# Kernel tuning notes

Hardware: AMD Instinct MI355X
Metric: run time of the kernel (lower is better)

The kernel has to match this reference:

```python
import jax, jax.numpy as jnp
import numpy as np

B, C, D, H, W = 2, 384, 32, 32, 32
HEADS, WS = 12, 5
HD = C // HEADS
PAD = WS // 2
SCALE = HD ** -0.5


def setup_inputs() -> dict:
    key = jax.random.key(0)
    ks = jax.random.split(key, 6)
    return {
        "x": jax.random.normal(ks[0], (B, C, D, H, W), jnp.float32),
        "w_qkv": jax.random.normal(ks[1], (3 * C, C), jnp.float32) * 0.02,
        "b_qkv": jax.random.normal(ks[2], (3 * C,), jnp.float32) * 0.02,
        "w_proj": jax.random.normal(ks[3], (C, C), jnp.float32) * 0.02,
        "b_proj": jax.random.normal(ks[4], (C,), jnp.float32) * 0.02,
        "pos_embed": jax.random.normal(ks[5], (HD, WS, WS, WS), jnp.float32) * 0.02,
    }


def reference(x, w_qkv, b_qkv, w_proj, b_proj, pos_embed):
    # 1x1x1 conv == pointwise linear over channels
    qkv = jnp.einsum('bcdhw,oc->bodhw', x, w_qkv) + b_qkv[None, :, None, None, None]
    q, k, v = jnp.split(qkv, 3, axis=1)
    q = q.reshape(B, HEADS, HD, D, H, W)
    k = k.reshape(B, HEADS, HD, D, H, W)
    v = v.reshape(B, HEADS, HD, D, H, W)
    pad_cfg = ((0, 0), (0, 0), (0, 0), (PAD, PAD), (PAD, PAD), (PAD, PAD))
    k_pad = jnp.pad(k, pad_cfg)  # zero padding, as in torch F.pad(value=0)
    v_pad = jnp.pad(v, pad_cfg)
    # per-offset scores: equivalent to unfold(ws)^3 without materializing windows
    scores = []
    for dz in range(WS):
        for dy in range(WS):
            for dx in range(WS):
                k_s = k_pad[:, :, :, dz:dz + D, dy:dy + H, dx:dx + W]
                # pos embed is added to k windows (including padded zeros) as in original
                k_s = k_s + pos_embed[:, dz, dy, dx][None, None, :, None, None, None]
                scores.append(jnp.sum(q * k_s, axis=2) * SCALE)  # [B,heads,D,H,W]
    scores = jnp.stack(scores, axis=-1)  # [B,heads,D,H,W,WS^3]
    wts = jax.nn.softmax(scores, axis=-1)
    out = jnp.zeros((B, HEADS, HD, D, H, W), x.dtype)
    i = 0
    for dz in range(WS):
        for dy in range(WS):
            for dx in range(WS):
                v_s = v_pad[:, :, :, dz:dz + D, dy:dy + H, dx:dx + W]
                out = out + wts[..., i][:, :, None] * v_s
                i += 1
    out = out.reshape(B, C, D, H, W)
    out = jnp.einsum('bcdhw,oc->bodhw', out, w_proj) + b_proj[None, :, None, None, None]
    return out
```

## Files before the change

kernel.cpp:

```cpp
#include <hip/hip_runtime.h>


#define NB 2
#define NC 384
#define NHEADS 12
#define NHD 32
#define NS 32768
#define PERB 12582912
#define SCALE_F 0.17677669529663687f
#define LOG2E_F 1.4426950408889634f
#define SL_F (0.17677669529663687f * 1.4426950408889634f)

typedef unsigned short bfr;
typedef float floatx4 __attribute__((ext_vector_type(4)));
typedef float f32x4 __attribute__((ext_vector_type(4)));
typedef short bf16x8 __attribute__((ext_vector_type(8)));
typedef short short4v __attribute__((ext_vector_type(4)));

union B8 { floatx4 v; bfr h[8]; };

__device__ __forceinline__ float b2f(bfr u) {
    union { unsigned int i; float f; } v;
    v.i = (unsigned int)u << 16;
    return v.f;
}
__device__ __forceinline__ bfr f2b(float f) {
    union { float f; unsigned int i; } v;
    v.f = f;
    unsigned int x = v.i;
    return (bfr)((x + 0x7fffu + ((x >> 16) & 1u)) >> 16);
}

__global__ void fill_code(float* out, float code) {
    for (size_t i = (size_t)blockIdx.x*256 + threadIdx.x; i < (size_t)NB*PERB;
         i += (size_t)gridDim.x*256) out[i] = code;
}

__global__ __launch_bounds__(256) void qkv_mfma(
    const float* __restrict__ x, const float* __restrict__ w,
    const float* __restrict__ bias,
    bfr* __restrict__ qT, bfr* __restrict__ kT, bfr* __restrict__ vT, int b)
{
    __shared__ __attribute__((aligned(16))) bfr wl[128*40];
    __shared__ __attribute__((aligned(16))) bfr xl[128*40];
    __shared__ float bsh[128];
    const int tid  = threadIdx.x;
    const int lane = tid & 63;
    const int wave = tid >> 6;
    const int wo   = (wave & 1) * 64;
    const int wsq  = (wave >> 1) * 64;
    const int s0   = blockIdx.x * 128;
    const int o0   = blockIdx.y * 128;
    const int m16  = lane & 15;
    const int g    = lane >> 4;

    if (tid < 128) bsh[tid] = bias[o0 + tid];

    f32x4 acc[4][4];
    #pragma unroll
    for (int i = 0; i < 4; ++i)
        #pragma unroll
        for (int j = 0; j < 4; ++j) acc[i][j] = (f32x4){0.f, 0.f, 0.f, 0.f};

    for (int kc = 0; kc < 12; ++kc) {
        const int c0 = kc * 32;
        #pragma unroll
        for (int r = 0; r < 4; ++r) {
            const int idx = r*256 + tid;
            const int o   = idx >> 3;
            const int c4  = (idx & 7) * 4;
            floatx4 wv = *(const floatx4*)&w[(size_t)(o0 + o)*NC + c0 + c4];
            short4v t;
            t[0] = (short)f2b(wv[0]); t[1] = (short)f2b(wv[1]);
            t[2] = (short)f2b(wv[2]); t[3] = (short)f2b(wv[3]);
            *(short4v*)&wl[o*40 + c4] = t;
        }
        #pragma unroll
        for (int r = 0; r < 4; ++r) {
            const int idx = r*256 + tid;
            const int c   = idx >> 5;
            const int s4  = (idx & 31) * 4;
            floatx4 xv =
                *(const floatx4*)&x[((size_t)b*NC + c0 + c)*NS + s0 + s4];
            #pragma unroll
            for (int i = 0; i < 4; ++i) xl[(s4 + i)*40 + c] = f2b(xv[i]);
        }
        __syncthreads();
        bf16x8 af[4], bfg[4];
        #pragma unroll
        for (int i = 0; i < 4; ++i)
            af[i] = *(bf16x8*)&wl[(wo + i*16 + m16)*40 + g*8];
        #pragma unroll
        for (int j = 0; j < 4; ++j)
            bfg[j] = *(bf16x8*)&xl[(wsq + j*16 + m16)*40 + g*8];
        #pragma unroll
        for (int i = 0; i < 4; ++i)
            #pragma unroll
            for (int j = 0; j < 4; ++j)
                acc[i][j] = __builtin_amdgcn_mfma_f32_16x16x32_bf16(
                    af[i], bfg[j], acc[i][j], 0, 0, 0);
        __syncthreads();
    }

    const int tens = blockIdx.y / 3;
    bfr* dstT = (tens == 0) ? qT : ((tens == 1) ? kT : vT);
    const int remb = o0 - tens*NC;
    const int q4   = g * 4;
    #pragma unroll
    for (int i = 0; i < 4; ++i) {
        const int olb = wo + i*16 + q4;
        const int ob  = remb + olb;
        const int hh  = ob >> 5;
        const int cc  = ob & 31;
        #pragma unroll
        for (int j = 0; j < 4; ++j) {
            const int s = s0 + wsq + j*16 + m16;
            short4v t;
            #pragma unroll
            for (int r = 0; r < 4; ++r)
                t[r] = (short)f2b(acc[i][j][r] + bsh[olb + r]);
            *(short4v*)&dstT[((size_t)hh*NS + s)*NHD + cc] = t;
        }
    }
}

__global__ __launch_bounds__(256, 4) void attn3d(
    const bfr* __restrict__ qT, const bfr* __restrict__ kT,
    const bfr* __restrict__ vT, const float* __restrict__ pe,
    bfr* __restrict__ aT)
{
    __shared__ __attribute__((aligned(16))) unsigned char smem[40960];
    bfr (*kl)[40]   = reinterpret_cast<bfr(*)[40]>(smem);
    bfr (*vtl)[136] = reinterpret_cast<bfr(*)[136]>(smem + 10240);
    bfr (*pel)[40]  = reinterpret_cast<bfr(*)[40]>(smem);
    bfr (*ql)[40]   = reinterpret_cast<bfr(*)[40]>(smem + 18944);
    bfr (*qpl)[132] = reinterpret_cast<bfr(*)[132]>(smem + 24064);

    const int tid  = threadIdx.x;
    const int lane = tid & 63;
    const int wave = tid >> 6;
    const int m16  = lane & 15;
    const int g    = lane >> 4;
    const int g4   = g << 2;
    const int bx   = blockIdx.x;
    const int tz = bx >> 6, ty = (bx >> 3) & 7, tx = bx & 7;
    const size_t hb = (size_t)blockIdx.y * NS;

    {
        const int qr = tid >> 2, part = tid & 3;
        const int qzr = qr >> 4, qyr = (qr >> 2) & 3, qxr = qr & 3;
        const size_t sq =
            (size_t)(tz*4 + qzr)*1024 + (ty*4 + qyr)*32 + (tx*4 + qxr);
        *(floatx4*)&ql[qr][part*8] =
            *(const floatx4*)&qT[(hb + sq)*NHD + part*8];
    }
    for (int e = tid; e < 4000; e += 256) {
        const int hd = e / 125;
        const int n  = e - hd*125;
        pel[n][hd] = f2b(pe[e]);
    }
    if (tid < 96) pel[125 + (tid >> 5)][tid & 31] = 0;
    __syncthreads();

    const int wq = wave*16 + m16;
    const bf16x8 bq = *(const bf16x8*)&ql[wq][g*8];

    #pragma unroll
    for (int t = 0; t < 8; ++t) {
        bf16x8 pa = *(const bf16x8*)&pel[t*16 + m16][g*8];
        f32x4 qa = __builtin_amdgcn_mfma_f32_16x16x32_bf16(
            pa, bq, (f32x4){0.f, 0.f, 0.f, 0.f}, 0, 0, 0);
        const unsigned w0 = (unsigned)f2b(qa[0]*SL_F) |
                            ((unsigned)f2b(qa[1]*SL_F) << 16);
        const unsigned w1 = (unsigned)f2b(qa[2]*SL_F) |
                            ((unsigned)f2b(qa[3]*SL_F) << 16);
        *(uint2*)&qpl[wq][t*16 + g4] = make_uint2(w0, w1);
    }
    if (g == 0) qpl[wq][128] = 0xFF80u;

    const int qy = m16 >> 2, qx = m16 & 3;
    unsigned nopk[4];
    #pragma unroll
    for (int tt = 0; tt < 4; ++tt) {
        unsigned v = 0;
        #pragma unroll
        for (int r = 0; r < 4; ++r) {
            const int t0 = g4 + r;
            const int hy = 2*tt + (t0 >> 3), hx = t0 & 7;
            const int dy = hy - qy, dx = hx - qx;
            const bool ok = ((unsigned)dy < 5u) && ((unsigned)dx < 5u);
            v |= (unsigned)(ok ? (dy*5 + dx) : 128) << (8*r);
        }
        nopk[tt] = v;
    }
    const bfr* qprow = qpl[wq];
    const int a0 = (m16 + 32*(g & 1)) * 4;
    const int a1 = a0 + 64;
    const bool ghi = (g >= 2);

    float m = -1e30f, l = 0.f;
    f32x4 o[2];
    o[0] = (f32x4){0.f, 0.f, 0.f, 0.f};
    o[1] = (f32x4){0.f, 0.f, 0.f, 0.f};

    for (int c = 0; c < 4; ++c) {
        __syncthreads();
        #pragma unroll
        for (int r2 = 0; r2 < 2; ++r2) {
            const int idx = r2*256 + tid;
            const int key = idx >> 2, part = idx & 3;
            const int hz = key >> 6, hy = (key >> 3) & 7, hx = key & 7;
            const int gz = tz*4 - 2 + 2*c + hz, gy = ty*4 - 2 + hy,
                      gx = tx*4 - 2 + hx;
            floatx4 kv = (floatx4){0.f, 0.f, 0.f, 0.f};
            if ((unsigned)gz < 32u && (unsigned)gy < 32u && (unsigned)gx < 32u)
                kv = *(const floatx4*)
                     &kT[(hb + gz*1024 + gy*32 + gx)*NHD + part*8];
            *(floatx4*)&kl[key][part*8] = kv;
        }
        {
            const int kp = tid & 63, hdo = tid >> 6;
            const int aK = 2*kp;
            const int hz = aK >> 6;
            const int hy = (aK >> 3) & 7, hx = aK & 7;
            const int gz = tz*4 - 2 + 2*c + hz, gy = ty*4 - 2 + hy,
                      gx = tx*4 - 2 + hx;
            const bool vzy = ((unsigned)gz < 32u) && ((unsigned)gy < 32u);
            B8 va, vb;
            va.v = (floatx4){0.f, 0.f, 0.f, 0.f};
            vb.v = (floatx4){0.f, 0.f, 0.f, 0.f};
            const size_t gb = hb + gz*1024 + gy*32;
            if (vzy && (unsigned)gx < 32u)
                va.v = *(const floatx4*)&vT[(gb + gx)*NHD + hdo*8];
            if (vzy && (unsigned)(gx + 1) < 32u)
                vb.v = *(const floatx4*)&vT[(gb + gx + 1)*NHD + hdo*8];
            #pragma unroll
            for (int i = 0; i < 8; ++i) {
                const unsigned u = (unsigned)va.h[i] | ((unsigned)vb.h[i] << 16);
                *(unsigned*)&vtl[hdo*8 + i][aK] = u;
            }
        }
        __syncthreads();

        #pragma unroll
        for (int zl = 0; zl < 2; ++zl) {
            const int dz = 2*c + zl - wave;
            if ((unsigned)dz > 4u) continue;
            const int nz = dz * 25;
            f32x4 s[4];
            __builtin_amdgcn_s_setprio(1);
            #pragma unroll
            for (int tt = 0; tt < 4; ++tt) {
                bf16x8 ka = *(const bf16x8*)&kl[zl*64 + tt*16 + m16][g*8];
                s[tt] = __builtin_amdgcn_mfma_f32_16x16x32_bf16(
                    ka, bq, (f32x4){0.f, 0.f, 0.f, 0.f}, 0, 0, 0);
            }
            __builtin_amdgcn_s_setprio(0);
            float mx = -1e30f;
            #pragma unroll
            for (int tt = 0; tt < 4; ++tt) {
                #pragma unroll
                for (int r = 0; r < 4; ++r) {
                    const unsigned n =
                        min((unsigned)nz + ((nopk[tt] >> (8*r)) & 255u), 128u);
                    const float qb  = b2f(qprow[n]);
                    const float val = fmaf(s[tt][r], SL_F, qb);
                    s[tt][r] = val;
                    mx = fmaxf(mx, val);
                }
            }
            mx = fmaxf(mx, __shfl_xor(mx, 16));
            mx = fmaxf(mx, __shfl_xor(mx, 32));
            const float mn = fmaxf(m, mx);
            const float al = exp2f(m - mn);
            m = mn;
            float ls = 0.f;
            unsigned pk[4][2];
            #pragma unroll
            for (int tt = 0; tt < 4; ++tt) {
                const float p0 = exp2f(s[tt][0] - mn);
                const float p1 = exp2f(s[tt][1] - mn);
                const float p2 = exp2f(s[tt][2] - mn);
                const float p3 = exp2f(s[tt][3] - mn);
                ls += (p0 + p1) + (p2 + p3);
                pk[tt][0] = (unsigned)f2b(p0) | ((unsigned)f2b(p1) << 16);
                pk[tt][1] = (unsigned)f2b(p2) | ((unsigned)f2b(p3) << 16);
            }
            ls += __shfl_xor(ls, 16);
            ls += __shfl_xor(ls, 32);
            l = l * al + ls;
            #pragma unroll
            for (int i = 0; i < 4; ++i) { o[0][i] *= al; o[1][i] *= al; }
            #pragma unroll
            for (int ksl = 0; ksl < 2; ++ksl) {
                union { unsigned u[4]; bf16x8 v; } pb;
                #pragma unroll
                for (int w = 0; w < 4; ++w) {
                    const int ad = (w < 2) ? a0 : a1;
                    const int wi = w & 1;
                    const int lo = __builtin_amdgcn_ds_bpermute(
                        ad, (int)pk[2*ksl][wi]);
                    const int hi = __builtin_amdgcn_ds_bpermute(
                        ad, (int)pk[2*ksl + 1][wi]);
                    pb.u[w] = ghi ? (unsigned)hi : (unsigned)lo;
                }
                __builtin_amdgcn_s_setprio(1);
                #pragma unroll
                for (int mt = 0; mt < 2; ++mt) {
                    bf16x8 va = *(const bf16x8*)
                        &vtl[mt*16 + m16][zl*64 + ksl*32 + g*8];
                    o[mt] = __builtin_amdgcn_mfma_f32_16x16x32_bf16(
                        va, pb.v, o[mt], 0, 0, 0);
                }
                __builtin_amdgcn_s_setprio(0);
            }
        }
    }

    const float rl = 1.f / l;
    const size_t sq = (size_t)(tz*4 + wave)*1024 + (ty*4 + qy)*32 + (tx*4 + qx);
    #pragma unroll
    for (int mt = 0; mt < 2; ++mt) {
        const unsigned w0 = (unsigned)f2b(o[mt][0]*rl) |
                            ((unsigned)f2b(o[mt][1]*rl) << 16);
        const unsigned w1 = (unsigned)f2b(o[mt][2]*rl) |
                            ((unsigned)f2b(o[mt][3]*rl) << 16);
        *(uint2*)&aT[(hb + sq)*NHD + mt*16 + g4] = make_uint2(w0, w1);
    }
}

__global__ __launch_bounds__(256) void proj_mfma(
    const bfr* __restrict__ aT, const float* __restrict__ w,
    const float* __restrict__ bias, float* __restrict__ out)
{
    __shared__ __attribute__((aligned(16))) bfr wl[128*40];
    __shared__ __attribute__((aligned(16))) bfr xl[128*40];
    __shared__ float bsh[128];
    const int tid  = threadIdx.x;
    const int lane = tid & 63;
    const int wave = tid >> 6;
    const int wo   = (wave & 1) * 64;
    const int wsq  = (wave >> 1) * 64;
    const int s0   = blockIdx.x * 128;
    const int o0   = blockIdx.y * 128;
    const int m16  = lane & 15;
    const int g    = lane >> 4;

    if (tid < 128) bsh[tid] = bias[o0 + tid];

    f32x4 acc[4][4];
    #pragma unroll
    for (int i = 0; i < 4; ++i)
        #pragma unroll
        for (int j = 0; j < 4; ++j) acc[i][j] = (f32x4){0.f, 0.f, 0.f, 0.f};

    for (int kc = 0; kc < 12; ++kc) {
        const int c0 = kc * 32;
        #pragma unroll
        for (int r = 0; r < 4; ++r) {
            const int idx = r*256 + tid;
            const int o   = idx >> 3;
            const int c4  = (idx & 7) * 4;
            floatx4 wv = *(const floatx4*)&w[(size_t)(o0 + o)*NC + c0 + c4];
            short4v t;
            t[0] = (short)f2b(wv[0]); t[1] = (short)f2b(wv[1]);
            t[2] = (short)f2b(wv[2]); t[3] = (short)f2b(wv[3]);
            *(short4v*)&wl[o*40 + c4] = t;
        }
        #pragma unroll
        for (int r = 0; r < 2; ++r) {
            const int idx = r*256 + tid;
            const int s   = idx >> 2;
            const int gg  = idx & 3;
            *(floatx4*)&xl[s*40 + gg*8] =
                *(const floatx4*)&aT[((size_t)kc*NS + s0 + s)*NHD + gg*8];
        }
        __syncthreads();
        bf16x8 af[4], bfg[4];
        #pragma unroll
        for (int i = 0; i < 4; ++i)
            af[i] = *(bf16x8*)&wl[(wo + i*16 + m16)*40 + g*8];
        #pragma unroll
        for (int j = 0; j < 4; ++j)
            bfg[j] = *(bf16x8*)&xl[(wsq + j*16 + m16)*40 + g*8];
        #pragma unroll
        for (int i = 0; i < 4; ++i)
            #pragma unroll
            for (int j = 0; j < 4; ++j)
                acc[i][j] = __builtin_amdgcn_mfma_f32_16x16x32_bf16(
                    af[i], bfg[j], acc[i][j], 0, 0, 0);
        __syncthreads();
    }

    const int q4 = g * 4;
    #pragma unroll
    for (int i = 0; i < 4; ++i) {
        const int olb = wo + i*16 + q4;
        #pragma unroll
        for (int j = 0; j < 4; ++j) {
            const int s = s0 + wsq + j*16 + m16;
            #pragma unroll
            for (int r = 0; r < 4; ++r)
                out[(size_t)(o0 + olb + r)*NS + s] = acc[i][j][r] + bsh[olb + r];
        }
    }
}

extern "C" void kernel_launch(void* const* d_in, const int* in_sizes, int n_in,
                              void* d_out, int out_size, void* d_ws, size_t ws_size,
                              hipStream_t stream)
{
    const float* x      = (const float*)d_in[0];
    const float* w_qkv  = (const float*)d_in[1];
    const float* b_qkv  = (const float*)d_in[2];
    const float* w_proj = (const float*)d_in[3];
    const float* b_proj = (const float*)d_in[4];
    const float* pe     = (const float*)d_in[5];
    float* outp = (float*)d_out;

    const size_t NEED = (size_t)2 * PERB * sizeof(bfr);
    if (ws_size < NEED) {
        fill_code<<<2048, 256, 0, stream>>>(outp, (float)(ws_size >> 20));
        return;
    }

    bfr* qT = (bfr*)d_ws;
    bfr* vT = qT + PERB;

    for (int b = 0; b < NB; ++b) {
        bfr* kT = (bfr*)(outp + (size_t)b * PERB);
        bfr* aT = qT;
        qkv_mfma<<<dim3(256, 9, 1), 256, 0, stream>>>(
            x, w_qkv, b_qkv, qT, kT, vT, b);
        attn3d<<<dim3(512, 12, 1), 256, 0, stream>>>(qT, kT, vT, pe, aT);
        proj_mfma<<<dim3(256, 3, 1), 256, 0, stream>>>(
            aT, w_proj, b_proj, outp + (size_t)b * PERB);
    }
}
```

Baseline: 713.3 us.

## Prefetch K/V into registers, use hardware bf16 pack, swap grid order

Measured after the change: 724.2 us. About the same (+1.5%).

```diff
diff --git a/kernel.cpp b/kernel.cpp
--- a/kernel.cpp
+++ b/kernel.cpp
@@ -29,6 +29,11 @@
     v.f = f;
     unsigned int x = v.i;
     return (bfr)((x + 0x7fffu + ((x >> 16) & 1u)) >> 16);
+}
+__device__ __forceinline__ unsigned cvt_pk2(float lo, float hi) {
+    unsigned r;
+    asm("v_cvt_pk_bf16_f32 %0, %1, %2" : "=v"(r) : "v"(lo), "v"(hi));
+    return r;
 }
 
 __global__ void fill_code(float* out, float code) {
@@ -49,8 +54,8 @@
     const int wave = tid >> 6;
     const int wo   = (wave & 1) * 64;
     const int wsq  = (wave >> 1) * 64;
-    const int s0   = blockIdx.x * 128;
-    const int o0   = blockIdx.y * 128;
+    const int s0   = blockIdx.y * 128;
+    const int o0   = blockIdx.x * 128;
     const int m16  = lane & 15;
     const int g    = lane >> 4;
 
@@ -102,7 +107,7 @@
         __syncthreads();
     }
 
-    const int tens = blockIdx.y / 3;
+    const int tens = blockIdx.x / 3;
     bfr* dstT = (tens == 0) ? qT : ((tens == 1) ? kT : vT);
     const int remb = o0 - tens*NC;
     const int q4   = g * 4;
@@ -170,28 +175,25 @@
         bf16x8 pa = *(const bf16x8*)&pel[t*16 + m16][g*8];
         f32x4 qa = __builtin_amdgcn_mfma_f32_16x16x32_bf16(
             pa, bq, (f32x4){0.f, 0.f, 0.f, 0.f}, 0, 0, 0);
-        const unsigned w0 = (unsigned)f2b(qa[0]*SL_F) |
-                            ((unsigned)f2b(qa[1]*SL_F) << 16);
-        const unsigned w1 = (unsigned)f2b(qa[2]*SL_F) |
-                            ((unsigned)f2b(qa[3]*SL_F) << 16);
+        const unsigned w0 = cvt_pk2(qa[0]*SL_F, qa[1]*SL_F);
+        const unsigned w1 = cvt_pk2(qa[2]*SL_F, qa[3]*SL_F);
         *(uint2*)&qpl[wq][t*16 + g4] = make_uint2(w0, w1);
     }
-    if (g == 0) qpl[wq][128] = 0xFF80u;
 
     const int qy = m16 >> 2, qx = m16 & 3;
-    unsigned nopk[4];
+    int   noff[16];
+    float maskf[16];
     #pragma unroll
     for (int tt = 0; tt < 4; ++tt) {
-        unsigned v = 0;
         #pragma unroll
         for (int r = 0; r < 4; ++r) {
             const int t0 = g4 + r;
             const int hy = 2*tt + (t0 >> 3), hx = t0 & 7;
             const int dy = hy - qy, dx = hx - qx;
             const bool ok = ((unsigned)dy < 5u) && ((unsigned)dx < 5u);
-            v |= (unsigned)(ok ? (dy*5 + dx) : 128) << (8*r);
-        }
-        nopk[tt] = v;
+            noff[tt*4 + r]  = ok ? (dy*5 + dx) : 0;
+            maskf[tt*4 + r] = ok ? 1.f : 0.f;
+        }
     }
     const bfr* qprow = qpl[wq];
     const int a0 = (m16 + 32*(g & 1)) * 4;
@@ -203,50 +205,60 @@
     o[0] = (f32x4){0.f, 0.f, 0.f, 0.f};
     o[1] = (f32x4){0.f, 0.f, 0.f, 0.f};
 
+    const int kkey0 = tid >> 2, kpart = tid & 3;
+    const int kkey1 = kkey0 + 64;
+    const int vkp   = tid & 63, vhdo = tid >> 6;
+    const int vaK   = 2*vkp;
+    floatx4 kst0, kst1;
+    B8 vsa, vsb;
+
+    auto kload = [&](int key, int c) -> floatx4 {
+        const int hz = key >> 6, hy = (key >> 3) & 7, hx = key & 7;
+        const int gz = tz*4 - 2 + 2*c + hz, gy = ty*4 - 2 + hy,
+                  gx = tx*4 - 2 + hx;
+        if ((unsigned)gz < 32u && (unsigned)gy < 32u && (unsigned)gx < 32u)
+            return *(const floatx4*)
+                   &kT[(hb + gz*1024 + gy*32 + gx)*NHD + kpart*8];
+        return (floatx4){0.f, 0.f, 0.f, 0.f};
+    };
+    auto vload = [&](int c) {
+        const int hz = vaK >> 6, hy = (vaK >> 3) & 7, hx = vaK & 7;
+        const int gz = tz*4 - 2 + 2*c + hz, gy = ty*4 - 2 + hy,
+                  gx = tx*4 - 2 + hx;
+        const bool vzy = ((unsigned)gz < 32u) && ((unsigned)gy < 32u);
+        vsa.v = (floatx4){0.f, 0.f, 0.f, 0.f};
+        vsb.v = (floatx4){0.f, 0.f, 0.f, 0.f};
+        const size_t gb = hb + gz*1024 + gy*32;
+        if (vzy && (unsigned)gx < 32u)
+            vsa.v = *(const floatx4*)&vT[(gb + gx)*NHD + vhdo*8];
+        if (vzy && (unsigned)(gx + 1) < 32u)
+            vsb.v = *(const floatx4*)&vT[(gb + gx + 1)*NHD + vhdo*8];
+    };
+
+    kst0 = kload(kkey0, 0);
+    kst1 = kload(kkey1, 0);
+    vload(0);
+
     for (int c = 0; c < 4; ++c) {
         __syncthreads();
-        #pragma unroll
-        for (int r2 = 0; r2 < 2; ++r2) {
-            const int idx = r2*256 + tid;
-            const int key = idx >> 2, part = idx & 3;
-            const int hz = key >> 6, hy = (key >> 3) & 7, hx = key & 7;
-            const int gz = tz*4 - 2 + 2*c + hz, gy = ty*4 - 2 + hy,
-                      gx = tx*4 - 2 + hx;
-            floatx4 kv = (floatx4){0.f, 0.f, 0.f, 0.f};
-            if ((unsigned)gz < 32u && (unsigned)gy < 32u && (unsigned)gx < 32u)
-                kv = *(const floatx4*)
-                     &kT[(hb + gz*1024 + gy*32 + gx)*NHD + part*8];
-            *(floatx4*)&kl[key][part*8] = kv;
-        }
-        {
-            const int kp = tid & 63, hdo = tid >> 6;
-            const int aK = 2*kp;
-            const int hz = aK >> 6;
-            const int hy = (aK >> 3) & 7, hx = aK & 7;
-            const int gz = tz*4 - 2 + 2*c + hz, gy = ty*4 - 2 + hy,
-                      gx = tx*4 - 2 + hx;
-            const bool vzy = ((unsigned)gz < 32u) && ((unsigned)gy < 32u);
-            B8 va, vb;
-            va.v = (floatx4){0.f, 0.f, 0.f, 0.f};
-            vb.v = (floatx4){0.f, 0.f, 0.f, 0.f};
-            const size_t gb = hb + gz*1024 + gy*32;
-            if (vzy && (unsigned)gx < 32u)
-                va.v = *(const floatx4*)&vT[(gb + gx)*NHD + hdo*8];
-            if (vzy && (unsigned)(gx + 1) < 32u)
-                vb.v = *(const floatx4*)&vT[(gb + gx + 1)*NHD + hdo*8];
-            #pragma unroll
-            for (int i = 0; i < 8; ++i) {
-                const unsigned u = (unsigned)va.h[i] | ((unsigned)vb.h[i] << 16);
-                *(unsigned*)&vtl[hdo*8 + i][aK] = u;
-            }
-        }
-        __syncthreads();
+        *(floatx4*)&kl[kkey0][kpart*8] = kst0;
+        *(floatx4*)&kl[kkey1][kpart*8] = kst1;
+        #pragma unroll
+        for (int i = 0; i < 8; ++i) {
+            const unsigned u = (unsigned)vsa.h[i] | ((unsigned)vsb.h[i] << 16);
+            *(unsigned*)&vtl[vhdo*8 + i][vaK] = u;
+        }
+        __syncthreads();
+        if (c < 3) {
+            kst0 = kload(kkey0, c + 1);
+            kst1 = kload(kkey1, c + 1);
+            vload(c + 1);
+        }
 
         #pragma unroll
         for (int zl = 0; zl < 2; ++zl) {
             const int dz = 2*c + zl - wave;
             if ((unsigned)dz > 4u) continue;
-            const int nz = dz * 25;
             f32x4 s[4];
             __builtin_amdgcn_s_setprio(1);
             #pragma unroll
@@ -256,18 +268,16 @@
                     ka, bq, (f32x4){0.f, 0.f, 0.f, 0.f}, 0, 0, 0);
             }
             __builtin_amdgcn_s_setprio(0);
+            const bfr* qb_l = qprow + dz*25;
             float mx = -1e30f;
             #pragma unroll
             for (int tt = 0; tt < 4; ++tt) {
-                #pragma unroll
-                for (int r = 0; r < 4; ++r) {
-                    const unsigned n =
-                        min((unsigned)nz + ((nopk[tt] >> (8*r)) & 255u), 128u);
-                    const float qb  = b2f(qprow[n]);
-                    const float val = fmaf(s[tt][r], SL_F, qb);
-                    s[tt][r] = val;
-                    mx = fmaxf(mx, val);
-                }
+                const float v0 = fmaf(s[tt][0], SL_F, b2f(qb_l[noff[tt*4+0]]));
+                const float v1 = fmaf(s[tt][1], SL_F, b2f(qb_l[noff[tt*4+1]]));
+                const float v2 = fmaf(s[tt][2], SL_F, b2f(qb_l[noff[tt*4+2]]));
+                const float v3 = fmaf(s[tt][3], SL_F, b2f(qb_l[noff[tt*4+3]]));
+                s[tt][0] = v0; s[tt][1] = v1; s[tt][2] = v2; s[tt][3] = v3;
+                mx = fmaxf(fmaxf(fmaxf(v0, v1), fmaxf(v2, v3)), mx);
             }
             mx = fmaxf(mx, __shfl_xor(mx, 16));
             mx = fmaxf(mx, __shfl_xor(mx, 32));
@@ -278,13 +288,13 @@
             unsigned pk[4][2];
             #pragma unroll
             for (int tt = 0; tt < 4; ++tt) {
-                const float p0 = exp2f(s[tt][0] - mn);
-                const float p1 = exp2f(s[tt][1] - mn);
-                const float p2 = exp2f(s[tt][2] - mn);
-                const float p3 = exp2f(s[tt][3] - mn);
+                const float p0 = exp2f(s[tt][0] - mn) * maskf[tt*4+0];
+                const float p1 = exp2f(s[tt][1] - mn) * maskf[tt*4+1];
+                const float p2 = exp2f(s[tt][2] - mn) * maskf[tt*4+2];
+                const float p3 = exp2f(s[tt][3] - mn) * maskf[tt*4+3];
                 ls += (p0 + p1) + (p2 + p3);
-                pk[tt][0] = (unsigned)f2b(p0) | ((unsigned)f2b(p1) << 16);
-                pk[tt][1] = (unsigned)f2b(p2) | ((unsigned)f2b(p3) << 16);
+                pk[tt][0] = cvt_pk2(p0, p1);
+                pk[tt][1] = cvt_pk2(p2, p3);
             }
             ls += __shfl_xor(ls, 16);
             ls += __shfl_xor(ls, 32);
@@ -321,10 +331,8 @@
     const size_t sq = (size_t)(tz*4 + wave)*1024 + (ty*4 + qy)*32 + (tx*4 + qx);
     #pragma unroll
     for (int mt = 0; mt < 2; ++mt) {
-        const unsigned w0 = (unsigned)f2b(o[mt][0]*rl) |
-                            ((unsigned)f2b(o[mt][1]*rl) << 16);
-        const unsigned w1 = (unsigned)f2b(o[mt][2]*rl) |
-                            ((unsigned)f2b(o[mt][3]*rl) << 16);
+        const unsigned w0 = cvt_pk2(o[mt][0]*rl, o[mt][1]*rl);
+        const unsigned w1 = cvt_pk2(o[mt][2]*rl, o[mt][3]*rl);
         *(uint2*)&aT[(hb + sq)*NHD + mt*16 + g4] = make_uint2(w0, w1);
     }
 }
@@ -341,8 +349,8 @@
     const int wave = tid >> 6;
     const int wo   = (wave & 1) * 64;
     const int wsq  = (wave >> 1) * 64;
-    const int s0   = blockIdx.x * 128;
-    const int o0   = blockIdx.y * 128;
+    const int s0   = blockIdx.y * 128;
+    const int o0   = blockIdx.x * 128;
     const int m16  = lane & 15;
     const int g    = lane >> 4;
 
@@ -430,10 +438,10 @@
     for (int b = 0; b < NB; ++b) {
         bfr* kT = (bfr*)(outp + (size_t)b * PERB);
         bfr* aT = qT;
-        qkv_mfma<<<dim3(256, 9, 1), 256, 0, stream>>>(
+        qkv_mfma<<<dim3(9, 256, 1), 256, 0, stream>>>(
             x, w_qkv, b_qkv, qT, kT, vT, b);
         attn3d<<<dim3(512, 12, 1), 256, 0, stream>>>(qT, kT, vT, pe, aT);
-        proj_mfma<<<dim3(256, 3, 1), 256, 0, stream>>>(
+        proj_mfma<<<dim3(3, 256, 1), 256, 0, stream>>>(
             aT, w_proj, b_proj, outp + (size_t)b * PERB);
     }
 }
```

## Use hardware bf16 pack conversion, lazy softmax rescale, and swap GEMM grid order

Applied to the files above, without the earlier changes.

Result: no change. 699.8 us (-1.9%).

```diff
diff --git a/kernel.cpp b/kernel.cpp
--- a/kernel.cpp
+++ b/kernel.cpp
@@ -29,6 +29,11 @@
     v.f = f;
     unsigned int x = v.i;
     return (bfr)((x + 0x7fffu + ((x >> 16) & 1u)) >> 16);
+}
+__device__ __forceinline__ unsigned cvt_pk2(float lo, float hi) {
+    unsigned r;
+    asm("v_cvt_pk_bf16_f32 %0, %1, %2" : "=v"(r) : "v"(lo), "v"(hi));
+    return r;
 }
 
 __global__ void fill_code(float* out, float code) {
@@ -49,8 +54,8 @@
     const int wave = tid >> 6;
     const int wo   = (wave & 1) * 64;
     const int wsq  = (wave >> 1) * 64;
-    const int s0   = blockIdx.x * 128;
-    const int o0   = blockIdx.y * 128;
+    const int s0   = blockIdx.y * 128;
+    const int o0   = blockIdx.x * 128;
     const int m16  = lane & 15;
     const int g    = lane >> 4;
 
@@ -70,10 +75,8 @@
             const int o   = idx >> 3;
             const int c4  = (idx & 7) * 4;
             floatx4 wv = *(const floatx4*)&w[(size_t)(o0 + o)*NC + c0 + c4];
-            short4v t;
-            t[0] = (short)f2b(wv[0]); t[1] = (short)f2b(wv[1]);
-            t[2] = (short)f2b(wv[2]); t[3] = (short)f2b(wv[3]);
-            *(short4v*)&wl[o*40 + c4] = t;
+            *(uint2*)&wl[o*40 + c4] =
+                make_uint2(cvt_pk2(wv[0], wv[1]), cvt_pk2(wv[2], wv[3]));
         }
         #pragma unroll
         for (int r = 0; r < 4; ++r) {
@@ -102,7 +105,7 @@
         __syncthreads();
     }
 
-    const int tens = blockIdx.y / 3;
+    const int tens = blockIdx.x / 3;
     bfr* dstT = (tens == 0) ? qT : ((tens == 1) ? kT : vT);
     const int remb = o0 - tens*NC;
     const int q4   = g * 4;
@@ -115,11 +118,11 @@
         #pragma unroll
         for (int j = 0; j < 4; ++j) {
             const int s = s0 + wsq + j*16 + m16;
-            short4v t;
-            #pragma unroll
-            for (int r = 0; r < 4; ++r)
-                t[r] = (short)f2b(acc[i][j][r] + bsh[olb + r]);
-            *(short4v*)&dstT[((size_t)hh*NS + s)*NHD + cc] = t;
+            const unsigned u0 = cvt_pk2(acc[i][j][0] + bsh[olb + 0],
+                                        acc[i][j][1] + bsh[olb + 1]);
+            const unsigned u1 = cvt_pk2(acc[i][j][2] + bsh[olb + 2],
+                                        acc[i][j][3] + bsh[olb + 3]);
+            *(uint2*)&dstT[((size_t)hh*NS + s)*NHD + cc] = make_uint2(u0, u1);
         }
     }
 }
@@ -170,10 +173,8 @@
         bf16x8 pa = *(const bf16x8*)&pel[t*16 + m16][g*8];
         f32x4 qa = __builtin_amdgcn_mfma_f32_16x16x32_bf16(
             pa, bq, (f32x4){0.f, 0.f, 0.f, 0.f}, 0, 0, 0);
-        const unsigned w0 = (unsigned)f2b(qa[0]*SL_F) |
-                            ((unsigned)f2b(qa[1]*SL_F) << 16);
-        const unsigned w1 = (unsigned)f2b(qa[2]*SL_F) |
-                            ((unsigned)f2b(qa[3]*SL_F) << 16);
+        const unsigned w0 = cvt_pk2(qa[0]*SL_F, qa[1]*SL_F);
+        const unsigned w1 = cvt_pk2(qa[2]*SL_F, qa[3]*SL_F);
         *(uint2*)&qpl[wq][t*16 + g4] = make_uint2(w0, w1);
     }
     if (g == 0) qpl[wq][128] = 0xFF80u;
@@ -272,25 +273,28 @@
             mx = fmaxf(mx, __shfl_xor(mx, 16));
             mx = fmaxf(mx, __shfl_xor(mx, 32));
             const float mn = fmaxf(m, mx);
-            const float al = exp2f(m - mn);
-            m = mn;
+            if (__any(mx > m)) {
+                const float al = exp2f(m - mn);
+                l *= al;
+                #pragma unroll
+                for (int i = 0; i < 4; ++i) { o[0][i] *= al; o[1][i] *= al; }
+                m = mn;
+            }
             float ls = 0.f;
             unsigned pk[4][2];
             #pragma unroll
             for (int tt = 0; tt < 4; ++tt) {
-                const float p0 = exp2f(s[tt][0] - mn);
-                const float p1 = exp2f(s[tt][1] - mn);
-                const float p2 = exp2f(s[tt][2] - mn);
-                const float p3 = exp2f(s[tt][3] - mn);
+                const float p0 = exp2f(s[tt][0] - m);
+                const float p1 = exp2f(s[tt][1] - m);
+                const float p2 = exp2f(s[tt][2] - m);
+                const float p3 = exp2f(s[tt][3] - m);
                 ls += (p0 + p1) + (p2 + p3);
-                pk[tt][0] = (unsigned)f2b(p0) | ((unsigned)f2b(p1) << 16);
-                pk[tt][1] = (unsigned)f2b(p2) | ((unsigned)f2b(p3) << 16);
+                pk[tt][0] = cvt_pk2(p0, p1);
+                pk[tt][1] = cvt_pk2(p2, p3);
             }
             ls += __shfl_xor(ls, 16);
             ls += __shfl_xor(ls, 32);
-            l = l * al + ls;
-            #pragma unroll
-            for (int i = 0; i < 4; ++i) { o[0][i] *= al; o[1][i] *= al; }
+            l += ls;
             #pragma unroll
             for (int ksl = 0; ksl < 2; ++ksl) {
                 union { unsigned u[4]; bf16x8 v; } pb;
@@ -321,10 +325,8 @@
     const size_t sq = (size_t)(tz*4 + wave)*1024 + (ty*4 + qy)*32 + (tx*4 + qx);
     #pragma unroll
     for (int mt = 0; mt < 2; ++mt) {
-        const unsigned w0 = (unsigned)f2b(o[mt][0]*rl) |
-                            ((unsigned)f2b(o[mt][1]*rl) << 16);
-        const unsigned w1 = (unsigned)f2b(o[mt][2]*rl) |
-                            ((unsigned)f2b(o[mt][3]*rl) << 16);
+        const unsigned w0 = cvt_pk2(o[mt][0]*rl, o[mt][1]*rl);
+        const unsigned w1 = cvt_pk2(o[mt][2]*rl, o[mt][3]*rl);
         *(uint2*)&aT[(hb + sq)*NHD + mt*16 + g4] = make_uint2(w0, w1);
     }
 }
@@ -341,8 +343,8 @@
     const int wave = tid >> 6;
     const int wo   = (wave & 1) * 64;
     const int wsq  = (wave >> 1) * 64;
-    const int s0   = blockIdx.x * 128;
-    const int o0   = blockIdx.y * 128;
+    const int s0   = blockIdx.y * 128;
+    const int o0   = blockIdx.x * 128;
     const int m16  = lane & 15;
     const int g    = lane >> 4;
 
@@ -362,10 +364,8 @@
             const int o   = idx >> 3;
             const int c4  = (idx & 7) * 4;
             floatx4 wv = *(const floatx4*)&w[(size_t)(o0 + o)*NC + c0 + c4];
-            short4v t;
-            t[0] = (short)f2b(wv[0]); t[1] = (short)f2b(wv[1]);
-            t[2] = (short)f2b(wv[2]); t[3] = (short)f2b(wv[3]);
-            *(short4v*)&wl[o*40 + c4] = t;
+            *(uint2*)&wl[o*40 + c4] =
+                make_uint2(cvt_pk2(wv[0], wv[1]), cvt_pk2(wv[2], wv[3]));
         }
         #pragma unroll
         for (int r = 0; r < 2; ++r) {
@@ -430,10 +430,10 @@
     for (int b = 0; b < NB; ++b) {
         bfr* kT = (bfr*)(outp + (size_t)b * PERB);
         bfr* aT = qT;
-        qkv_mfma<<<dim3(256, 9, 1), 256, 0, stream>>>(
+        qkv_mfma<<<dim3(9, 256, 1), 256, 0, stream>>>(
             x, w_qkv, b_qkv, qT, kT, vT, b);
         attn3d<<<dim3(512, 12, 1), 256, 0, stream>>>(qT, kT, vT, pe, aT);
-        proj_mfma<<<dim3(256, 3, 1), 256, 0, stream>>>(
+        proj_mfma<<<dim3(3, 256, 1), 256, 0, stream>>>(
             aT, w_proj, b_proj, outp + (size_t)b * PERB);
     }
 }
```
